# Kernel optimization log

Hardware: AMD Instinct MI355X
Metric: run time of the kernel (lower is better)

The kernel has to match this reference:

```python
import jax, jax.numpy as jnp
import numpy as np

EPS = 1e-5

def _layernorm(x, gamma, beta, axes):
    mean = jnp.mean(x, axis=axes, keepdims=True)
    var = jnp.var(x, axis=axes, keepdims=True)
    return (x - mean) * jax.lax.rsqrt(var + EPS) * gamma + beta

def setup_inputs() -> dict:
    key = jax.random.key(0)
    ks = jax.random.split(key, 14)
    B, N1, N2, D1, D2 = 128, 32, 32, 23, 13
    E, H, F = 72, 256, 128
    N = N1 + N2
    s = 0.05
    return {
        "x_a": jax.random.normal(ks[0], (B, N1, D1), jnp.float32),
        "x_b": jax.random.normal(ks[1], (B, N2, D2), jnp.float32),
        "W_a": jax.random.normal(ks[2], (D1, E), jnp.float32) * s,
        "b_a": jnp.zeros((E,), jnp.float32),
        "W_b": jax.random.normal(ks[3], (D2, E), jnp.float32) * s,
        "b_b": jnp.zeros((E,), jnp.float32),
        "ln0_g": jnp.ones((N, E), jnp.float32),
        "ln0_b": jnp.zeros((N, E), jnp.float32),
        "W_g": jax.random.normal(ks[4], (2 * E, H), jnp.float32) * s,
        "b_g": jnp.zeros((H,), jnp.float32),
        "lng_g": jnp.ones((H,), jnp.float32),
        "lng_b": jnp.zeros((H,), jnp.float32),
        "W_f": jax.random.normal(ks[5], (H, F), jnp.float32) * s,
        "b_f": jnp.zeros((F,), jnp.float32),
    }

def reference(x_a, x_b, W_a, b_a, W_b, b_b, ln0_g, ln0_b,
              W_g, b_g, lng_g, lng_b, W_f, b_f):
    # SplitEmbedding: per-group linear embed, concat along entity dim
    a = jnp.concatenate([x_a @ W_a + b_a, x_b @ W_b + b_b], axis=-2)  # [B, N, E]
    # LayerNorm over last two dims (num_entities, embed_dim) jointly
    a = _layernorm(a, ln0_g, ln0_b, axes=(-2, -1))
    B, N, E = a.shape
    # ij(): aij[b, i, j] = concat(a[b, i], a[b, j])  -> [B, N, N, 2E]
    ai = jnp.broadcast_to(a[:, :, None, :], (B, N, N, E))
    aj = jnp.broadcast_to(a[:, None, :, :], (B, N, N, E))
    aij = jnp.concatenate([ai, aj], axis=-1)
    # g: Linear(2E, H) + ELU, then LayerNorm(H)
    g = jax.nn.elu(aij @ W_g + b_g)  # [B, N, N, H]
    g = _layernorm(g, lng_g, lng_b, axes=(-1,))
    # sum over both pairwise dims
    s = jnp.sum(g, axis=(-3, -2))  # [B, H]
    # f: Linear(H, F) + ELU
    return jax.nn.elu(s @ W_f + b_f)  # [B, F]
```

## Files before the change

### kernel.cpp

```cpp
#include <hip/hip_runtime.h>
#include <hip/hip_bf16.h>

#define EPS 1e-5f

#define OFF_ABAR 0
#define OFF_U    589824
#define OFF_V    2686976
#define OFF_PART 4784128

__device__ __forceinline__ float elu(float z) {
    return z > 0.f ? z : __expf(z) - 1.f;
}

__global__ __launch_bounds__(256) void k_embed_ln0(
    const float* __restrict__ xa, const float* __restrict__ xb,
    const float* __restrict__ Wa, const float* __restrict__ ba,
    const float* __restrict__ Wb, const float* __restrict__ bb,
    const float* __restrict__ g0, const float* __restrict__ b0,
    float* __restrict__ abar) {
    int b = blockIdx.x;
    int tid = threadIdx.x;
    float vals[18];
    float s1 = 0.f, s2 = 0.f;
    for (int m = 0; m < 18; ++m) {
        int k = tid + 256 * m;
        int e = k % 72;
        int n = k / 72;
        float acc;
        if (n < 32) {
            acc = ba[e];
            const float* x = xa + (b * 32 + n) * 23;
            #pragma unroll
            for (int d = 0; d < 23; ++d) acc = fmaf(x[d], Wa[d * 72 + e], acc);
        } else {
            acc = bb[e];
            const float* x = xb + (b * 32 + (n - 32)) * 13;
            #pragma unroll
            for (int d = 0; d < 13; ++d) acc = fmaf(x[d], Wb[d * 72 + e], acc);
        }
        vals[m] = acc;
        s1 += acc;
        s2 = fmaf(acc, acc, s2);
    }
    #pragma unroll
    for (int off = 32; off >= 1; off >>= 1) {
        s1 += __shfl_xor(s1, off, 64);
        s2 += __shfl_xor(s2, off, 64);
    }
    __shared__ float r1[4], r2[4];
    int w = tid >> 6;
    if ((tid & 63) == 0) { r1[w] = s1; r2[w] = s2; }
    __syncthreads();
    float t1 = r1[0] + r1[1] + r1[2] + r1[3];
    float t2 = r2[0] + r2[1] + r2[2] + r2[3];
    float mean = t1 * (1.f / 4608.f);
    float var  = fmaf(-mean, mean, t2 * (1.f / 4608.f));
    float rsq  = rsqrtf(var + EPS);
    float* ab = abar + b * 4608;
    for (int m = 0; m < 18; ++m) {
        int k = tid + 256 * m;
        ab[k] = fmaf((vals[m] - mean) * rsq, g0[k], b0[k]);
    }
}

__global__ __launch_bounds__(256) void k_uv(
    const float* __restrict__ abar, const float* __restrict__ Wg,
    const float* __restrict__ bg,
    float* __restrict__ U, float* __restrict__ V) {
    int blk = blockIdx.x;
    int b = blk >> 2;
    int q = blk & 3;
    int h = threadIdx.x;
    __shared__ float sa[72 * 16];
    const float* src = abar + (b * 64 + q * 16) * 72;
    for (int k = threadIdx.x; k < 72 * 16; k += 256) {
        int e = k >> 4, n = k & 15;
        sa[k] = src[n * 72 + e];
    }
    __syncthreads();
    float u[16], v[16];
    #pragma unroll
    for (int n = 0; n < 16; ++n) { u[n] = 0.f; v[n] = 0.f; }
    for (int e = 0; e < 72; ++e) {
        float wu = Wg[e * 256 + h];
        float wv = Wg[(72 + e) * 256 + h];
        const float4* sp = (const float4*)&sa[e * 16];
        #pragma unroll
        for (int n4 = 0; n4 < 4; ++n4) {
            float4 s4 = sp[n4];
            u[n4*4+0] = fmaf(s4.x, wu, u[n4*4+0]); v[n4*4+0] = fmaf(s4.x, wv, v[n4*4+0]);
            u[n4*4+1] = fmaf(s4.y, wu, u[n4*4+1]); v[n4*4+1] = fmaf(s4.y, wv, v[n4*4+1]);
            u[n4*4+2] = fmaf(s4.z, wu, u[n4*4+2]); v[n4*4+2] = fmaf(s4.z, wv, v[n4*4+2]);
            u[n4*4+3] = fmaf(s4.w, wu, u[n4*4+3]); v[n4*4+3] = fmaf(s4.w, wv, v[n4*4+3]);
        }
    }
    float bgh = bg[h];
    int base = (b * 64 + q * 16) * 256 + h;
    #pragma unroll
    for (int n = 0; n < 16; ++n) {
        U[base + n * 256] = u[n] + bgh;
        V[base + n * 256] = v[n];
    }
}

__global__ __launch_bounds__(256, 8) void k_pair(
    const float* __restrict__ U, const float* __restrict__ V,
    float* __restrict__ part) {
    int blk = blockIdx.x;
    int b  = blk >> 4;
    int iq = (blk >> 2) & 3;
    int jq = blk & 3;
    int t  = threadIdx.x;
    int j16 = t >> 4;
    int hc  = t & 15;
    int w   = t >> 6;

    __shared__ float Us[16 * 256];
    __shared__ float Sc[4 * 256];

    const float* Ug = U + (size_t)(b * 64 + iq * 16) * 256;
    #pragma unroll
    for (int r = 0; r < 4; ++r) {
        int k = t * 4 + r * 1024;
        *(float4*)&Us[k] = *(const float4*)&Ug[k];
    }

    const float* Vrow = V + (size_t)(b * 64 + jq * 16 + j16) * 256;
    float v[16];
    #pragma unroll
    for (int c = 0; c < 4; ++c) {
        float4 v4 = *(const float4*)&Vrow[hc * 4 + 64 * c];
        v[c*4+0] = v4.x; v[c*4+1] = v4.y; v[c*4+2] = v4.z; v[c*4+3] = v4.w;
    }

    __syncthreads();

    float acc[16];
    #pragma unroll
    for (int k = 0; k < 16; ++k) acc[k] = 0.f;
    float macc = 0.f;

    for (int i = 0; i < 16; ++i) {
        const float* ur = &Us[i * 256];
        float e[16];
        float s1 = 0.f, s2 = 0.f;
        #pragma unroll
        for (int c = 0; c < 4; ++c) {
            float4 u4 = *(const float4*)&ur[hc * 4 + 64 * c];
            float e0 = elu(u4.x + v[c*4+0]);
            float e1 = elu(u4.y + v[c*4+1]);
            float e2 = elu(u4.z + v[c*4+2]);
            float e3 = elu(u4.w + v[c*4+3]);
            e[c*4+0] = e0; e[c*4+1] = e1; e[c*4+2] = e2; e[c*4+3] = e3;
            s1 += (e0 + e1) + (e2 + e3);
            s2 = fmaf(e0, e0, fmaf(e1, e1, fmaf(e2, e2, fmaf(e3, e3, s2))));
        }
        #pragma unroll
        for (int d = 1; d <= 8; d <<= 1) {
            s1 += __shfl_xor(s1, d, 64);
            s2 += __shfl_xor(s2, d, 64);
        }
        float mu  = s1 * (1.f / 256.f);
        float var = fmaf(-mu, mu, s2 * (1.f / 256.f));
        float rsq = rsqrtf(var + EPS);
        macc += mu * rsq;
        #pragma unroll
        for (int k = 0; k < 16; ++k) acc[k] = fmaf(e[k], rsq, acc[k]);
    }
    #pragma unroll
    for (int k = 0; k < 16; ++k) acc[k] -= macc;

    #pragma unroll
    for (int d = 16; d <= 32; d <<= 1) {
        #pragma unroll
        for (int k = 0; k < 16; ++k) acc[k] += __shfl_xor(acc[k], d, 64);
    }
    if ((t & 63) < 16) {
        #pragma unroll
        for (int c = 0; c < 4; ++c)
            *(float4*)&Sc[w * 256 + hc * 4 + 64 * c] =
                make_float4(acc[c*4+0], acc[c*4+1], acc[c*4+2], acc[c*4+3]);
    }
    __syncthreads();
    float r = Sc[t] + Sc[256 + t] + Sc[512 + t] + Sc[768 + t];
    part[(size_t)blk * 256 + t] = r;
}

__global__ __launch_bounds__(128) void k_out(
    const float* __restrict__ part,
    const float* __restrict__ lgg, const float* __restrict__ lgb,
    const float* __restrict__ Wf,  const float* __restrict__ bfb,
    float* __restrict__ out) {
    int b = blockIdx.x;
    int f = threadIdx.x;
    __shared__ float sh[256];
    for (int h = f; h < 256; h += 128) {
        float s = 0.f;
        #pragma unroll
        for (int p = 0; p < 16; ++p) s += part[(size_t)(b * 16 + p) * 256 + h];
        sh[h] = fmaf(lgg[h], s, 4096.f * lgb[h]);
    }
    __syncthreads();
    float acc = bfb[f];
    for (int h = 0; h < 256; ++h)
        acc = fmaf(sh[h], Wf[h * 128 + f], acc);
    float r = acc > 0.f ? acc : __expf(acc) - 1.f;
    out[b * 128 + f] = r;
}

extern "C" void kernel_launch(void* const* d_in, const int* in_sizes, int n_in,
                              void* d_out, int out_size, void* d_ws, size_t ws_size,
                              hipStream_t stream) {
    const float* xa  = (const float*)d_in[0];
    const float* xb  = (const float*)d_in[1];
    const float* Wa  = (const float*)d_in[2];
    const float* ba  = (const float*)d_in[3];
    const float* Wb  = (const float*)d_in[4];
    const float* bb  = (const float*)d_in[5];
    const float* g0  = (const float*)d_in[6];
    const float* b0  = (const float*)d_in[7];
    const float* Wg  = (const float*)d_in[8];
    const float* bg  = (const float*)d_in[9];
    const float* lgg = (const float*)d_in[10];
    const float* lgb = (const float*)d_in[11];
    const float* Wf  = (const float*)d_in[12];
    const float* bfb = (const float*)d_in[13];
    float* out = (float*)d_out;

    float* ws   = (float*)d_ws;
    float* abar = ws + OFF_ABAR;
    float* U    = ws + OFF_U;
    float* V    = ws + OFF_V;
    float* part = ws + OFF_PART;

    k_embed_ln0<<<128, 256, 0, stream>>>(xa, xb, Wa, ba, Wb, bb, g0, b0, abar);
    k_uv<<<512, 256, 0, stream>>>(abar, Wg, bg, U, V);
    k_pair<<<2048, 256, 0, stream>>>(U, V, part);
    k_out<<<128, 128, 0, stream>>>(part, lgg, lgb, Wf, bfb, out);
}
```

Measured before the change: 158.4 us.

## Use DPP row reductions, reuse Us for block reduce, split k_uv and k_out work

The 16-lane LayerNorm reductions in k_pair now use DPP row_shr adds instead of ds_swizzle shuffles. The cross-wave accumulation reuses the Us shared buffer and does a 16-way sum, which drops the xor shuffles on 16 accumulators. The launch-bounds occupancy hint drops from 8 to 6. k_uv processes 8 entities per block over 1024 blocks for more parallelism, and k_out splits the Wf matvec across 256 threads. The DPP row_shr sequence leaves only the last lane of each 16-lane row holding the full sum, so other lanes get partial statistics, which risks wrong results.

```diff
diff --git a/kernel.cpp b/kernel.cpp
--- a/kernel.cpp
+++ b/kernel.cpp
@@ -10,6 +10,19 @@
 
 __device__ __forceinline__ float elu(float z) {
     return z > 0.f ? z : __expf(z) - 1.f;
+}
+
+template <int CTRL>
+__device__ __forceinline__ float dpp_add(float x) {
+    int y = __builtin_amdgcn_update_dpp(0, __float_as_int(x), CTRL, 0xf, 0xf, true);
+    return x + __int_as_float(y);
+}
+__device__ __forceinline__ float allred16(float x) {
+    x = dpp_add<0x121>(x);
+    x = dpp_add<0x122>(x);
+    x = dpp_add<0x124>(x);
+    x = dpp_add<0x128>(x);
+    return x;
 }
 
 __global__ __launch_bounds__(256) void k_embed_ln0(
@@ -68,25 +81,25 @@
     const float* __restrict__ bg,
     float* __restrict__ U, float* __restrict__ V) {
     int blk = blockIdx.x;
-    int b = blk >> 2;
-    int q = blk & 3;
+    int b = blk >> 3;
+    int q = blk & 7;
     int h = threadIdx.x;
-    __shared__ float sa[72 * 16];
-    const float* src = abar + (b * 64 + q * 16) * 72;
-    for (int k = threadIdx.x; k < 72 * 16; k += 256) {
-        int e = k >> 4, n = k & 15;
+    __shared__ float sa[72 * 8];
+    const float* src = abar + (b * 64 + q * 8) * 72;
+    for (int k = threadIdx.x; k < 72 * 8; k += 256) {
+        int e = k >> 3, n = k & 7;
         sa[k] = src[n * 72 + e];
     }
     __syncthreads();
-    float u[16], v[16];
-    #pragma unroll
-    for (int n = 0; n < 16; ++n) { u[n] = 0.f; v[n] = 0.f; }
+    float u[8], v[8];
+    #pragma unroll
+    for (int n = 0; n < 8; ++n) { u[n] = 0.f; v[n] = 0.f; }
     for (int e = 0; e < 72; ++e) {
         float wu = Wg[e * 256 + h];
         float wv = Wg[(72 + e) * 256 + h];
-        const float4* sp = (const float4*)&sa[e * 16];
-        #pragma unroll
-        for (int n4 = 0; n4 < 4; ++n4) {
+        const float4* sp = (const float4*)&sa[e * 8];
+        #pragma unroll
+        for (int n4 = 0; n4 < 2; ++n4) {
             float4 s4 = sp[n4];
             u[n4*4+0] = fmaf(s4.x, wu, u[n4*4+0]); v[n4*4+0] = fmaf(s4.x, wv, v[n4*4+0]);
             u[n4*4+1] = fmaf(s4.y, wu, u[n4*4+1]); v[n4*4+1] = fmaf(s4.y, wv, v[n4*4+1]);
@@ -95,15 +108,15 @@
         }
     }
     float bgh = bg[h];
-    int base = (b * 64 + q * 16) * 256 + h;
-    #pragma unroll
-    for (int n = 0; n < 16; ++n) {
+    int base = (b * 64 + q * 8) * 256 + h;
+    #pragma unroll
+    for (int n = 0; n < 8; ++n) {
         U[base + n * 256] = u[n] + bgh;
         V[base + n * 256] = v[n];
     }
 }
 
-__global__ __launch_bounds__(256, 8) void k_pair(
+__global__ __launch_bounds__(256, 6) void k_pair(
     const float* __restrict__ U, const float* __restrict__ V,
     float* __restrict__ part) {
     int blk = blockIdx.x;
@@ -113,10 +126,8 @@
     int t  = threadIdx.x;
     int j16 = t >> 4;
     int hc  = t & 15;
-    int w   = t >> 6;
 
     __shared__ float Us[16 * 256];
-    __shared__ float Sc[4 * 256];
 
     const float* Ug = U + (size_t)(b * 64 + iq * 16) * 256;
     #pragma unroll
@@ -155,11 +166,8 @@
             s1 += (e0 + e1) + (e2 + e3);
             s2 = fmaf(e0, e0, fmaf(e1, e1, fmaf(e2, e2, fmaf(e3, e3, s2))));
         }
-        #pragma unroll
-        for (int d = 1; d <= 8; d <<= 1) {
-            s1 += __shfl_xor(s1, d, 64);
-            s2 += __shfl_xor(s2, d, 64);
-        }
+        s1 = allred16(s1);
+        s2 = allred16(s2);
         float mu  = s1 * (1.f / 256.f);
         float var = fmaf(-mu, mu, s2 * (1.f / 256.f));
         float rsq = rsqrtf(var + EPS);
@@ -170,42 +178,44 @@
     #pragma unroll
     for (int k = 0; k < 16; ++k) acc[k] -= macc;
 
-    #pragma unroll
-    for (int d = 16; d <= 32; d <<= 1) {
-        #pragma unroll
-        for (int k = 0; k < 16; ++k) acc[k] += __shfl_xor(acc[k], d, 64);
-    }
-    if ((t & 63) < 16) {
-        #pragma unroll
-        for (int c = 0; c < 4; ++c)
-            *(float4*)&Sc[w * 256 + hc * 4 + 64 * c] =
-                make_float4(acc[c*4+0], acc[c*4+1], acc[c*4+2], acc[c*4+3]);
-    }
-    __syncthreads();
-    float r = Sc[t] + Sc[256 + t] + Sc[512 + t] + Sc[768 + t];
+    __syncthreads();
+    #pragma unroll
+    for (int c = 0; c < 4; ++c)
+        *(float4*)&Us[j16 * 256 + hc * 4 + 64 * c] =
+            make_float4(acc[c*4+0], acc[c*4+1], acc[c*4+2], acc[c*4+3]);
+    __syncthreads();
+    float r = 0.f;
+    #pragma unroll
+    for (int q = 0; q < 16; ++q) r += Us[q * 256 + t];
     part[(size_t)blk * 256 + t] = r;
 }
 
-__global__ __launch_bounds__(128) void k_out(
+__global__ __launch_bounds__(256) void k_out(
     const float* __restrict__ part,
     const float* __restrict__ lgg, const float* __restrict__ lgb,
     const float* __restrict__ Wf,  const float* __restrict__ bfb,
     float* __restrict__ out) {
     int b = blockIdx.x;
-    int f = threadIdx.x;
+    int t = threadIdx.x;
     __shared__ float sh[256];
-    for (int h = f; h < 256; h += 128) {
+    __shared__ float ps[256];
+    {
         float s = 0.f;
         #pragma unroll
-        for (int p = 0; p < 16; ++p) s += part[(size_t)(b * 16 + p) * 256 + h];
-        sh[h] = fmaf(lgg[h], s, 4096.f * lgb[h]);
-    }
-    __syncthreads();
-    float acc = bfb[f];
-    for (int h = 0; h < 256; ++h)
+        for (int p = 0; p < 16; ++p) s += part[(size_t)(b * 16 + p) * 256 + t];
+        sh[t] = fmaf(lgg[t], s, 4096.f * lgb[t]);
+    }
+    __syncthreads();
+    int f = t & 127, half = t >> 7;
+    float acc = 0.f;
+    for (int h = half * 128; h < half * 128 + 128; ++h)
         acc = fmaf(sh[h], Wf[h * 128 + f], acc);
-    float r = acc > 0.f ? acc : __expf(acc) - 1.f;
-    out[b * 128 + f] = r;
+    ps[t] = acc;
+    __syncthreads();
+    if (t < 128) {
+        float r = ps[t] + ps[t + 128] + bfb[t];
+        out[b * 128 + t] = r > 0.f ? r : __expf(r) - 1.f;
+    }
 }
 
 extern "C" void kernel_launch(void* const* d_in, const int* in_sizes, int n_in,
@@ -234,7 +244,7 @@
     float* part = ws + OFF_PART;
 
     k_embed_ln0<<<128, 256, 0, stream>>>(xa, xb, Wa, ba, Wb, bb, g0, b0, abar);
-    k_uv<<<512, 256, 0, stream>>>(abar, Wg, bg, U, V);
+    k_uv<<<1024, 256, 0, stream>>>(abar, Wg, bg, U, V);
     k_pair<<<2048, 256, 0, stream>>>(U, V, part);
-    k_out<<<128, 128, 0, stream>>>(part, lgg, lgb, Wf, bfb, out);
-}
+    k_out<<<128, 256, 0, stream>>>(part, lgg, lgb, Wf, bfb, out);
+}
```

After: 178.0 us. 12.4% more time.
